# Kernel tuning notes

Hardware: AMD Instinct MI355X
Metric: run time of the kernel (lower is better)

Reference implementation:

```python
import jax, jax.numpy as jnp
import numpy as np

N, D, P, T, M, H = 8192, 64, 32, 1, 50, 512
INTERVAL = 1.0
SIGMA = 1.0


def setup_inputs() -> dict:
    key = jax.random.key(0)
    k = jax.random.split(key, 9)
    in_dim = 1 + D + P  # [s, X, Y_t]
    return {
        "X0": jax.random.normal(k[0], (N, D), jnp.float32),
        "V0": jax.random.normal(k[1], (N,), jnp.float32),
        "Y": jax.random.normal(k[2], (N, T, P), jnp.float32),
        "theta": jax.random.normal(k[3], (D,), jnp.float32),
        "W1": jax.random.normal(k[4], (in_dim, H), jnp.float32) / np.sqrt(in_dim),
        "b1": jnp.zeros((H,), jnp.float32),
        "W2": jax.random.normal(k[5], (H, D), jnp.float32) / np.sqrt(H),
        "b2": jnp.zeros((D,), jnp.float32),
        "noise": jax.random.normal(k[6], (M, N, D), jnp.float32),
        "obs_index": 0,
    }


def reference(X0, V0, Y, theta, W1, b1, W2, b2, noise, obs_index):
    dt = jnp.float32(INTERVAL / M)
    sqrt_dt = jnp.sqrt(dt)
    Yt = Y[:, obs_index, :]  # (N, p) observation at this index

    def z_net(s, X):
        # Z_net(t, s, X, Y): MLP over [s, X, Y_t] -> (N, d)
        s_col = jnp.full((X.shape[0], 1), s, X.dtype)
        h = jnp.tanh(jnp.concatenate([s_col, X, Yt], axis=1) @ W1 + b1)
        return h @ W2 + b2

    def step(carry, xs):
        X, V = carry
        s, w = xs
        Wm = sqrt_dt * w  # Brownian increment
        Z = z_net(s, X)
        control = -jax.lax.stop_gradient(Z)  # -Z.detach()
        drift_V = 0.5 * jnp.sum(Z * Z, axis=1) + jnp.sum(control * Z, axis=1)
        V_new = V + dt * drift_V + jnp.sum(Z * Wm, axis=1)
        drift_X = (theta - X) + SIGMA * control  # b(theta, X) = theta - X (OU)
        X_new = X + dt * drift_X + SIGMA * Wm
        return (X_new, V_new), None

    times = jnp.arange(M, dtype=X0.dtype) * dt
    (X, V), _ = jax.lax.scan(step, (X0, V0), (times, noise))
    return X, V
```

## Files before the change

kernel.cpp:

```cpp
#include <hip/hip_runtime.h>
#include <hip/hip_bf16.h>

typedef __attribute__((ext_vector_type(4))) float f32x4;
typedef __attribute__((ext_vector_type(8))) short bf16x8;

#define NPART 8192
#define DDIM 64
#define PDIM 32
#define MSTEPS 50
#define HDIM 512
#define W1T_LD 72
#define H_LD 520

__device__ __forceinline__ short f2bf(float f) {
  unsigned u = __builtin_bit_cast(unsigned, f);
  u = (u + 0x7fffu + ((u >> 16) & 1u)) >> 16;
  return (short)u;
}

__device__ __forceinline__ float fast_tanh(float xv) {
  float t = __expf(2.0f * xv);
  return 1.0f - 2.0f * __builtin_amdgcn_rcpf(t + 1.0f);
}

__global__ __launch_bounds__(512) void sde_kernel(
    const float* __restrict__ X0, const float* __restrict__ V0,
    const float* __restrict__ Y, const float* __restrict__ theta,
    const float* __restrict__ W1, const float* __restrict__ b1,
    const float* __restrict__ W2, const float* __restrict__ b2,
    const float* __restrict__ noise, const int* __restrict__ obs_index,
    float* __restrict__ out) {
  __shared__ __align__(16) short lds_w1t[HDIM * W1T_LD];
  __shared__ __align__(16) short lds_a[32 * W1T_LD];
  __shared__ __align__(16) short lds_h[32 * H_LD];
  __shared__ float lds_vp[32 * 4];
  __shared__ float lds_v[32];

  const int tid = threadIdx.x;
  const int w = tid >> 6;
  const int lane = tid & 63;
  const int c = lane & 15;
  const int g = lane >> 4;
  const int pb = blockIdx.x * 32;

  const float dt = 0.02f;
  const float sqdt = sqrtf(dt);

  {
    const int n = tid;
    const float* src = W1 + 512 + n;
    #pragma unroll
    for (int k2 = 0; k2 < 32; ++k2) {
      float a0 = src[(2 * k2) * 512];
      float a1 = src[(2 * k2 + 1) * 512];
      unsigned pk = (unsigned)(unsigned short)f2bf(a0) |
                    ((unsigned)(unsigned short)f2bf(a1) << 16);
      *reinterpret_cast<int*>(&lds_w1t[n * W1T_LD + 2 * k2]) = pk;
    }
  }

  {
    float* yt = reinterpret_cast<float*>(lds_h);
    const int obs = obs_index[0];
    for (int i = tid; i < 32 * PDIM; i += 512) {
      int m = i >> 5, p = i & 31;
      yt[i] = Y[((size_t)(pb + m) * 1 + obs) * PDIM + p];
    }
  }

  const int mtw = w >> 2, ntw = w & 3;
  float x[4];
  #pragma unroll
  for (int r = 0; r < 4; ++r) {
    int m = 16 * mtw + 4 * g + r;
    x[r] = X0[(size_t)(pb + m) * DDIM + 16 * ntw + c];
    lds_a[m * W1T_LD + 16 * ntw + c] = f2bf(x[r]);
  }
  if (tid < 32) lds_v[tid] = V0[pb + tid];

  __syncthreads();

  float cy[2][4][4];
  float rv0[4];
  int nj[4];
  #pragma unroll
  for (int j = 0; j < 4; ++j) {
    nj[j] = 64 * w + 16 * j + c;
    rv0[j] = W1[nj[j]];
    float bv = b1[nj[j]];
    #pragma unroll
    for (int mt = 0; mt < 2; ++mt)
      #pragma unroll
      for (int r = 0; r < 4; ++r) cy[mt][j][r] = bv;
  }
  {
    const float* yt = reinterpret_cast<const float*>(lds_h);
    for (int p = 0; p < PDIM; ++p) {
      float wv[4];
      #pragma unroll
      for (int j = 0; j < 4; ++j) wv[j] = W1[(65 + p) * 512 + nj[j]];
      #pragma unroll
      for (int mt = 0; mt < 2; ++mt) {
        #pragma unroll
        for (int r = 0; r < 4; ++r) {
          float yv = yt[(16 * mt + 4 * g + r) * PDIM + p];
          #pragma unroll
          for (int j = 0; j < 4; ++j) cy[mt][j][r] = fmaf(yv, wv[j], cy[mt][j][r]);
        }
      }
    }
  }

  bf16x8 w2f[16];
  #pragma unroll
  for (int kt = 0; kt < 16; ++kt) {
    #pragma unroll
    for (int i = 0; i < 8; ++i) {
      w2f[kt][i] = f2bf(W2[(size_t)(32 * kt + 8 * g + i) * DDIM + 16 * ntw + c]);
    }
  }
  const float thv = theta[16 * ntw + c];
  const float b2v = b2[16 * ntw + c];

  __syncthreads();

  for (int st = 0; st < MSTEPS; ++st) {
    const float s = st * dt;

    float wm[4];
    const float* np_ = noise + ((size_t)st * NPART + pb) * DDIM + 16 * ntw + c;
    #pragma unroll
    for (int r = 0; r < 4; ++r) wm[r] = np_[(size_t)(16 * mtw + 4 * g + r) * DDIM];

    f32x4 acc1[2][4];
    #pragma unroll
    for (int mt = 0; mt < 2; ++mt)
      #pragma unroll
      for (int j = 0; j < 4; ++j) acc1[mt][j] = (f32x4){0.f, 0.f, 0.f, 0.f};

    bf16x8 af[2][2], bfr[4][2];
    #pragma unroll
    for (int mt = 0; mt < 2; ++mt)
      #pragma unroll
      for (int kt = 0; kt < 2; ++kt)
        af[mt][kt] = *reinterpret_cast<const bf16x8*>(
            &lds_a[(16 * mt + c) * W1T_LD + 32 * kt + 8 * g]);
    #pragma unroll
    for (int j = 0; j < 4; ++j)
      #pragma unroll
      for (int kt = 0; kt < 2; ++kt)
        bfr[j][kt] = *reinterpret_cast<const bf16x8*>(
            &lds_w1t[nj[j] * W1T_LD + 32 * kt + 8 * g]);

    #pragma unroll
    for (int mt = 0; mt < 2; ++mt)
      #pragma unroll
      for (int j = 0; j < 4; ++j)
        #pragma unroll
        for (int kt = 0; kt < 2; ++kt)
          acc1[mt][j] = __builtin_amdgcn_mfma_f32_16x16x32_bf16(
              af[mt][kt], bfr[j][kt], acc1[mt][j], 0, 0, 0);

    #pragma unroll
    for (int mt = 0; mt < 2; ++mt)
      #pragma unroll
      for (int j = 0; j < 4; ++j)
        #pragma unroll
        for (int r = 0; r < 4; ++r) {
          float pre = acc1[mt][j][r] + cy[mt][j][r] + s * rv0[j];
          float h = fast_tanh(pre);
          lds_h[(16 * mt + 4 * g + r) * H_LD + nj[j]] = f2bf(h);
        }

    __syncthreads();

    f32x4 acc2 = (f32x4){b2v, b2v, b2v, b2v};
    #pragma unroll
    for (int kt = 0; kt < 16; ++kt) {
      bf16x8 ha = *reinterpret_cast<const bf16x8*>(
          &lds_h[(16 * mtw + c) * H_LD + 32 * kt + 8 * g]);
      acc2 = __builtin_amdgcn_mfma_f32_16x16x32_bf16(ha, w2f[kt], acc2, 0, 0, 0);
    }

    float vr[4];
    #pragma unroll
    for (int r = 0; r < 4; ++r) {
      float z = acc2[r];
      float wmr = sqdt * wm[r];
      vr[r] = z * (wmr - 0.5f * dt * z);
      x[r] = x[r] + dt * (thv - x[r] - z) + wmr;
    }
    #pragma unroll
    for (int mask = 1; mask <= 8; mask <<= 1)
      #pragma unroll
      for (int r = 0; r < 4; ++r) vr[r] += __shfl_xor(vr[r], mask);
    if (c == 0) {
      #pragma unroll
      for (int r = 0; r < 4; ++r)
        lds_vp[(16 * mtw + 4 * g + r) * 4 + ntw] = vr[r];
    }
    #pragma unroll
    for (int r = 0; r < 4; ++r)
      lds_a[(16 * mtw + 4 * g + r) * W1T_LD + 16 * ntw + c] = f2bf(x[r]);

    __syncthreads();

    if (tid < 32) {
      lds_v[tid] += lds_vp[tid * 4] + lds_vp[tid * 4 + 1] +
                    lds_vp[tid * 4 + 2] + lds_vp[tid * 4 + 3];
    }
  }

  #pragma unroll
  for (int r = 0; r < 4; ++r)
    out[(size_t)(pb + 16 * mtw + 4 * g + r) * DDIM + 16 * ntw + c] = x[r];
  if (tid < 32) out[(size_t)NPART * DDIM + pb + tid] = lds_v[tid];
}

extern "C" void kernel_launch(void* const* d_in, const int* in_sizes, int n_in,
                              void* d_out, int out_size, void* d_ws, size_t ws_size,
                              hipStream_t stream) {
  sde_kernel<<<256, 512, 0, stream>>>(
      (const float*)d_in[0], (const float*)d_in[1], (const float*)d_in[2],
      (const float*)d_in[3], (const float*)d_in[4], (const float*)d_in[5],
      (const float*)d_in[6], (const float*)d_in[7], (const float*)d_in[8],
      (const int*)d_in[9], (float*)d_out);
}
```

Measured before the change: 295.7 us.

## Double block to 1024 threads, split second GEMM over K and keep W1 in registers

```diff
diff --git a/kernel.cpp b/kernel.cpp
--- a/kernel.cpp
+++ b/kernel.cpp
@@ -9,7 +9,7 @@
 #define PDIM 32
 #define MSTEPS 50
 #define HDIM 512
-#define W1T_LD 72
+#define A_LD 72
 #define H_LD 520
 
 __device__ __forceinline__ short f2bf(float f) {
@@ -23,18 +23,25 @@
   return 1.0f - 2.0f * __builtin_amdgcn_rcpf(t + 1.0f);
 }
 
-__global__ __launch_bounds__(512) void sde_kernel(
+__device__ __forceinline__ unsigned pack_pair(float own) {
+  int oi = __builtin_amdgcn_mov_dpp(__builtin_bit_cast(int, own),
+                                    0xB1 , 0xF, 0xF, true);
+  float other = __builtin_bit_cast(float, oi);
+  unsigned out;
+  asm("v_cvt_pk_bf16_f32 %0, %1, %2" : "=v"(out) : "v"(own), "v"(other));
+  return out;
+}
+
+__global__ __launch_bounds__(1024) void sde_kernel(
     const float* __restrict__ X0, const float* __restrict__ V0,
     const float* __restrict__ Y, const float* __restrict__ theta,
     const float* __restrict__ W1, const float* __restrict__ b1,
     const float* __restrict__ W2, const float* __restrict__ b2,
     const float* __restrict__ noise, const int* __restrict__ obs_index,
     float* __restrict__ out) {
-  __shared__ __align__(16) short lds_w1t[HDIM * W1T_LD];
-  __shared__ __align__(16) short lds_a[32 * W1T_LD];
   __shared__ __align__(16) short lds_h[32 * H_LD];
-  __shared__ float lds_vp[32 * 4];
-  __shared__ float lds_v[32];
+  __shared__ __align__(16) short lds_a[32 * A_LD];
+  __shared__ __align__(16) float lds_p[8 * 64 * 4];
 
   const int tid = threadIdx.x;
   const int w = tid >> 6;
@@ -42,185 +49,173 @@
   const int c = lane & 15;
   const int g = lane >> 4;
   const int pb = blockIdx.x * 32;
+  const int kh = w & 1, ntw = (w >> 1) & 3, mtw = w >> 3;
 
   const float dt = 0.02f;
   const float sqdt = sqrtf(dt);
 
   {
-    const int n = tid;
-    const float* src = W1 + 512 + n;
-    #pragma unroll
-    for (int k2 = 0; k2 < 32; ++k2) {
-      float a0 = src[(2 * k2) * 512];
-      float a1 = src[(2 * k2 + 1) * 512];
-      unsigned pk = (unsigned)(unsigned short)f2bf(a0) |
-                    ((unsigned)(unsigned short)f2bf(a1) << 16);
-      *reinterpret_cast<int*>(&lds_w1t[n * W1T_LD + 2 * k2]) = pk;
-    }
-  }
-
+    int m = tid >> 5, p = tid & 31;
+    lds_p[m * PDIM + p] =
+        Y[(size_t)(pb + m) * PDIM + (size_t)obs_index[0] * PDIM + p];
+  }
+
+  float x[4] = {0.f, 0.f, 0.f, 0.f};
+  if (kh == 0) {
+    #pragma unroll
+    for (int r = 0; r < 4; ++r) {
+      int m = 16 * mtw + 4 * g + r;
+      x[r] = X0[(size_t)(pb + m) * DDIM + 16 * ntw + c];
+      lds_a[m * A_LD + 16 * ntw + c] = f2bf(x[r]);
+    }
+  }
+  __syncthreads();
+
+  const int nj0 = 32 * w + c;
+  float cy[2][2][4];
+  float rv0[2] = {W1[nj0], W1[nj0 + 16]};
   {
-    float* yt = reinterpret_cast<float*>(lds_h);
-    const int obs = obs_index[0];
-    for (int i = tid; i < 32 * PDIM; i += 512) {
-      int m = i >> 5, p = i & 31;
-      yt[i] = Y[((size_t)(pb + m) * 1 + obs) * PDIM + p];
-    }
-  }
-
-  const int mtw = w >> 2, ntw = w & 3;
-  float x[4];
-  #pragma unroll
-  for (int r = 0; r < 4; ++r) {
-    int m = 16 * mtw + 4 * g + r;
-    x[r] = X0[(size_t)(pb + m) * DDIM + 16 * ntw + c];
-    lds_a[m * W1T_LD + 16 * ntw + c] = f2bf(x[r]);
-  }
-  if (tid < 32) lds_v[tid] = V0[pb + tid];
-
-  __syncthreads();
-
-  float cy[2][4][4];
-  float rv0[4];
-  int nj[4];
-  #pragma unroll
-  for (int j = 0; j < 4; ++j) {
-    nj[j] = 64 * w + 16 * j + c;
-    rv0[j] = W1[nj[j]];
-    float bv = b1[nj[j]];
+    float bv0 = b1[nj0], bv1 = b1[nj0 + 16];
     #pragma unroll
     for (int mt = 0; mt < 2; ++mt)
       #pragma unroll
-      for (int r = 0; r < 4; ++r) cy[mt][j][r] = bv;
-  }
-  {
-    const float* yt = reinterpret_cast<const float*>(lds_h);
+      for (int r = 0; r < 4; ++r) { cy[mt][0][r] = bv0; cy[mt][1][r] = bv1; }
     for (int p = 0; p < PDIM; ++p) {
-      float wv[4];
-      #pragma unroll
-      for (int j = 0; j < 4; ++j) wv[j] = W1[(65 + p) * 512 + nj[j]];
-      #pragma unroll
-      for (int mt = 0; mt < 2; ++mt) {
+      float wv0 = W1[(size_t)(65 + p) * HDIM + nj0];
+      float wv1 = W1[(size_t)(65 + p) * HDIM + nj0 + 16];
+      #pragma unroll
+      for (int mt = 0; mt < 2; ++mt)
         #pragma unroll
         for (int r = 0; r < 4; ++r) {
-          float yv = yt[(16 * mt + 4 * g + r) * PDIM + p];
+          float yv = lds_p[(16 * mt + 4 * g + r) * PDIM + p];
+          cy[mt][0][r] = fmaf(yv, wv0, cy[mt][0][r]);
+          cy[mt][1][r] = fmaf(yv, wv1, cy[mt][1][r]);
+        }
+    }
+  }
+
+  bf16x8 bfr[2][2];
+  #pragma unroll
+  for (int e = 0; e < 2; ++e)
+    #pragma unroll
+    for (int kt = 0; kt < 2; ++kt)
+      #pragma unroll
+      for (int i = 0; i < 8; ++i)
+        bfr[e][kt][i] =
+            f2bf(W1[(size_t)(1 + 32 * kt + 8 * g + i) * HDIM + nj0 + 16 * e]);
+
+  bf16x8 w2f[8];
+  #pragma unroll
+  for (int kt = 0; kt < 8; ++kt)
+    #pragma unroll
+    for (int i = 0; i < 8; ++i)
+      w2f[kt][i] =
+          f2bf(W2[(size_t)(256 * kh + 32 * kt + 8 * g + i) * DDIM + 16 * ntw + c]);
+
+  const float thv = theta[16 * ntw + c];
+  const float b2v = b2[16 * ntw + c];
+  float vacc[4] = {0.f, 0.f, 0.f, 0.f};
+
+  __syncthreads();
+
+  for (int st = 0; st < MSTEPS; ++st) {
+    const float s = st * dt;
+
+    float wm[4];
+    if (kh == 0) {
+      const float* np_ =
+          noise + ((size_t)st * NPART + pb + 16 * mtw + 4 * g) * DDIM + 16 * ntw + c;
+      #pragma unroll
+      for (int r = 0; r < 4; ++r) wm[r] = np_[(size_t)r * DDIM];
+    }
+
+    #pragma unroll
+    for (int mt = 0; mt < 2; ++mt) {
+      const int abase = (16 * mt + c) * A_LD + 8 * g;
+      bf16x8 af0 = *reinterpret_cast<const bf16x8*>(&lds_a[abase]);
+      bf16x8 af1 = *reinterpret_cast<const bf16x8*>(&lds_a[abase + 32]);
+      #pragma unroll
+      for (int e = 0; e < 2; ++e) {
+        f32x4 acc = {0.f, 0.f, 0.f, 0.f};
+        acc = __builtin_amdgcn_mfma_f32_16x16x32_bf16(af0, bfr[e][0], acc, 0, 0, 0);
+        acc = __builtin_amdgcn_mfma_f32_16x16x32_bf16(af1, bfr[e][1], acc, 0, 0, 0);
+        float sb = s * rv0[e];
+        unsigned pk[4];
+        #pragma unroll
+        for (int r = 0; r < 4; ++r)
+          pk[r] = pack_pair(fast_tanh(acc[r] + cy[mt][e][r] + sb));
+        if (!(lane & 1)) {
           #pragma unroll
-          for (int j = 0; j < 4; ++j) cy[mt][j][r] = fmaf(yv, wv[j], cy[mt][j][r]);
+          for (int r = 0; r < 4; ++r)
+            *reinterpret_cast<unsigned*>(
+                &lds_h[(16 * mt + 4 * g + r) * H_LD + nj0 + 16 * e]) = pk[r];
         }
       }
     }
-  }
-
-  bf16x8 w2f[16];
-  #pragma unroll
-  for (int kt = 0; kt < 16; ++kt) {
-    #pragma unroll
-    for (int i = 0; i < 8; ++i) {
-      w2f[kt][i] = f2bf(W2[(size_t)(32 * kt + 8 * g + i) * DDIM + 16 * ntw + c]);
-    }
-  }
-  const float thv = theta[16 * ntw + c];
-  const float b2v = b2[16 * ntw + c];
-
+
+    __syncthreads();
+
+    f32x4 acc2 = {0.f, 0.f, 0.f, 0.f};
+    {
+      const int hbase = (16 * mtw + c) * H_LD + 256 * kh + 8 * g;
+      #pragma unroll
+      for (int kt = 0; kt < 8; ++kt)
+        acc2 = __builtin_amdgcn_mfma_f32_16x16x32_bf16(
+            *reinterpret_cast<const bf16x8*>(&lds_h[hbase + 32 * kt]), w2f[kt],
+            acc2, 0, 0, 0);
+    }
+    float* pslot = &lds_p[((mtw * 4 + ntw) * 64 + lane) * 4];
+    if (kh) *reinterpret_cast<f32x4*>(pslot) = acc2;
+
+    __syncthreads();
+
+    if (!kh) {
+      f32x4 part = *reinterpret_cast<const f32x4*>(pslot);
+      unsigned apk[4];
+      #pragma unroll
+      for (int r = 0; r < 4; ++r) {
+        float z = acc2[r] + part[r] + b2v;
+        float wmr = sqdt * wm[r];
+        vacc[r] = fmaf(z, wmr - 0.5f * dt * z, vacc[r]);
+        x[r] = x[r] + dt * (thv - x[r] - z) + wmr;
+        apk[r] = pack_pair(x[r]);
+      }
+      if (!(lane & 1)) {
+        #pragma unroll
+        for (int r = 0; r < 4; ++r)
+          *reinterpret_cast<unsigned*>(
+              &lds_a[(16 * mtw + 4 * g + r) * A_LD + 16 * ntw + c]) = apk[r];
+      }
+    }
+
+    __syncthreads();
+  }
+
+  if (!kh) {
+    #pragma unroll
+    for (int r = 0; r < 4; ++r)
+      out[(size_t)(pb + 16 * mtw + 4 * g + r) * DDIM + 16 * ntw + c] = x[r];
+    #pragma unroll
+    for (int mask = 1; mask <= 8; mask <<= 1)
+      #pragma unroll
+      for (int r = 0; r < 4; ++r) vacc[r] += __shfl_xor(vacc[r], mask);
+    if (c == 0) {
+      #pragma unroll
+      for (int r = 0; r < 4; ++r)
+        lds_p[(16 * mtw + 4 * g + r) * 4 + ntw] = vacc[r];
+    }
+  }
   __syncthreads();
-
-  for (int st = 0; st < MSTEPS; ++st) {
-    const float s = st * dt;
-
-    float wm[4];
-    const float* np_ = noise + ((size_t)st * NPART + pb) * DDIM + 16 * ntw + c;
-    #pragma unroll
-    for (int r = 0; r < 4; ++r) wm[r] = np_[(size_t)(16 * mtw + 4 * g + r) * DDIM];
-
-    f32x4 acc1[2][4];
-    #pragma unroll
-    for (int mt = 0; mt < 2; ++mt)
-      #pragma unroll
-      for (int j = 0; j < 4; ++j) acc1[mt][j] = (f32x4){0.f, 0.f, 0.f, 0.f};
-
-    bf16x8 af[2][2], bfr[4][2];
-    #pragma unroll
-    for (int mt = 0; mt < 2; ++mt)
-      #pragma unroll
-      for (int kt = 0; kt < 2; ++kt)
-        af[mt][kt] = *reinterpret_cast<const bf16x8*>(
-            &lds_a[(16 * mt + c) * W1T_LD + 32 * kt + 8 * g]);
-    #pragma unroll
-    for (int j = 0; j < 4; ++j)
-      #pragma unroll
-      for (int kt = 0; kt < 2; ++kt)
-        bfr[j][kt] = *reinterpret_cast<const bf16x8*>(
-            &lds_w1t[nj[j] * W1T_LD + 32 * kt + 8 * g]);
-
-    #pragma unroll
-    for (int mt = 0; mt < 2; ++mt)
-      #pragma unroll
-      for (int j = 0; j < 4; ++j)
-        #pragma unroll
-        for (int kt = 0; kt < 2; ++kt)
-          acc1[mt][j] = __builtin_amdgcn_mfma_f32_16x16x32_bf16(
-              af[mt][kt], bfr[j][kt], acc1[mt][j], 0, 0, 0);
-
-    #pragma unroll
-    for (int mt = 0; mt < 2; ++mt)
-      #pragma unroll
-      for (int j = 0; j < 4; ++j)
-        #pragma unroll
-        for (int r = 0; r < 4; ++r) {
-          float pre = acc1[mt][j][r] + cy[mt][j][r] + s * rv0[j];
-          float h = fast_tanh(pre);
-          lds_h[(16 * mt + 4 * g + r) * H_LD + nj[j]] = f2bf(h);
-        }
-
-    __syncthreads();
-
-    f32x4 acc2 = (f32x4){b2v, b2v, b2v, b2v};
-    #pragma unroll
-    for (int kt = 0; kt < 16; ++kt) {
-      bf16x8 ha = *reinterpret_cast<const bf16x8*>(
-          &lds_h[(16 * mtw + c) * H_LD + 32 * kt + 8 * g]);
-      acc2 = __builtin_amdgcn_mfma_f32_16x16x32_bf16(ha, w2f[kt], acc2, 0, 0, 0);
-    }
-
-    float vr[4];
-    #pragma unroll
-    for (int r = 0; r < 4; ++r) {
-      float z = acc2[r];
-      float wmr = sqdt * wm[r];
-      vr[r] = z * (wmr - 0.5f * dt * z);
-      x[r] = x[r] + dt * (thv - x[r] - z) + wmr;
-    }
-    #pragma unroll
-    for (int mask = 1; mask <= 8; mask <<= 1)
-      #pragma unroll
-      for (int r = 0; r < 4; ++r) vr[r] += __shfl_xor(vr[r], mask);
-    if (c == 0) {
-      #pragma unroll
-      for (int r = 0; r < 4; ++r)
-        lds_vp[(16 * mtw + 4 * g + r) * 4 + ntw] = vr[r];
-    }
-    #pragma unroll
-    for (int r = 0; r < 4; ++r)
-      lds_a[(16 * mtw + 4 * g + r) * W1T_LD + 16 * ntw + c] = f2bf(x[r]);
-
-    __syncthreads();
-
-    if (tid < 32) {
-      lds_v[tid] += lds_vp[tid * 4] + lds_vp[tid * 4 + 1] +
-                    lds_vp[tid * 4 + 2] + lds_vp[tid * 4 + 3];
-    }
-  }
-
-  #pragma unroll
-  for (int r = 0; r < 4; ++r)
-    out[(size_t)(pb + 16 * mtw + 4 * g + r) * DDIM + 16 * ntw + c] = x[r];
-  if (tid < 32) out[(size_t)NPART * DDIM + pb + tid] = lds_v[tid];
+  if (tid < 32)
+    out[(size_t)NPART * DDIM + pb + tid] =
+        V0[pb + tid] + lds_p[tid * 4] + lds_p[tid * 4 + 1] +
+        lds_p[tid * 4 + 2] + lds_p[tid * 4 + 3];
 }
 
 extern "C" void kernel_launch(void* const* d_in, const int* in_sizes, int n_in,
                               void* d_out, int out_size, void* d_ws, size_t ws_size,
                               hipStream_t stream) {
-  sde_kernel<<<256, 512, 0, stream>>>(
+  sde_kernel<<<256, 1024, 0, stream>>>(
       (const float*)d_in[0], (const float*)d_in[1], (const float*)d_in[2],
       (const float*)d_in[3], (const float*)d_in[4], (const float*)d_in[5],
       (const float*)d_in[6], (const float*)d_in[7], (const float*)d_in[8],
```

Result: faster. 272.5 us (-7.8%).
